# Optimization experiments

Measured on AMD Instinct MI355X. Metric: run time of the kernel, lower is better.

Reference implementation:

```python
import jax, jax.numpy as jnp
import numpy as np

BATCH, SEQ, DIM = 4, 4096, 1024


def setup_inputs() -> dict:
    key = jax.random.key(0)
    ks = jax.random.split(key, 7)
    return {
        "x": jax.random.normal(ks[0], (BATCH, SEQ, DIM), dtype=jnp.float32),
        "phazor_re": jax.random.normal(ks[1], (DIM,), dtype=jnp.float32),
        "phazor_im": jax.random.normal(ks[2], (DIM,), dtype=jnp.float32),
        "phazor_init_re": jax.random.normal(ks[3], (DIM,), dtype=jnp.float32),
        "phazor_init_im": jax.random.normal(ks[4], (DIM,), dtype=jnp.float32),
        "last_conv_re": jax.random.normal(ks[5], (BATCH, DIM), dtype=jnp.float32),
        "last_conv_im": jax.random.normal(ks[6], (BATCH, DIM), dtype=jnp.float32),
    }


def reference(x, phazor_re, phazor_im, phazor_init_re, phazor_init_im,
              last_conv_re, last_conv_im):
    L = x.shape[1]
    phazor_p = phazor_re + 1j * phazor_im                      # raw param (dim,)
    phazor_init = phazor_init_re + 1j * phazor_init_im          # (dim,)
    last_conv = last_conv_re + 1j * last_conv_im                # (batch, dim)

    mag = jnp.abs(phazor_p)
    phazor = phazor_p / mag * jnp.exp(-mag)                     # (dim,) |phazor|<1
    t = jnp.arange(L)[:, None]                                  # (L,1)
    phazor_prog = jnp.power(phazor[None, :], t)                 # (L, dim) = phazor^t
    filt = phazor_prog * phazor_init[None, :]                   # (L, dim)

    filt_fft = jnp.fft.fft(filt, n=2 * L, axis=0)               # (2L, dim)
    x_fft = jnp.fft.fft(x.astype(jnp.complex64), n=2 * L, axis=1)  # (B, 2L, dim)
    conv = jnp.fft.ifft(filt_fft[None] * x_fft, axis=1)[:, :L]  # (B, L, dim)

    # add decayed initial state: last_conv * phazor^(t+1)
    conv = conv + last_conv[:, None, :] * phazor_prog[None] * phazor[None, None, :]
    return conv.real
```

## Files before the change

kernel.cpp:

```cpp
#include <hip/hip_runtime.h>


#define BB 4
#define LL 4096
#define DD 1024
#define CHUNK 16
#define KK (LL / CHUNK)

__device__ __forceinline__ void phazor_of(float pr, float pi, float& ar, float& ai) {
    float mag = sqrtf(pr * pr + pi * pi);
    float s = expf(-mag) / mag;
    ar = pr * s;
    ai = pi * s;
}

__global__ __launch_bounds__(256, 4) void spiral_pass1(
    const float* __restrict__ x,
    const float* __restrict__ p_re, const float* __restrict__ p_im,
    const float* __restrict__ in_re, const float* __restrict__ in_im,
    float2* __restrict__ S)
{
    int tid = blockIdx.x * 256 + threadIdx.x;
    int dq = tid & (DD / 4 - 1);
    int k  = (tid >> 8) & (KK - 1);
    int b  = tid >> 16;
    int d0 = dq * 4;

    float4 prv = *(const float4*)(p_re + d0);
    float4 piv = *(const float4*)(p_im + d0);
    float4 brv = *(const float4*)(in_re + d0);
    float4 biv = *(const float4*)(in_im + d0);
    float ar[4], ai[4];
    float br[4] = {brv.x, brv.y, brv.z, brv.w};
    float bi[4] = {biv.x, biv.y, biv.z, biv.w};
    {
        float prs[4] = {prv.x, prv.y, prv.z, prv.w};
        float pis[4] = {piv.x, piv.y, piv.z, piv.w};
#pragma unroll
        for (int q = 0; q < 4; ++q) phazor_of(prs[q], pis[q], ar[q], ai[q]);
    }

    float sr[4] = {0.f, 0.f, 0.f, 0.f};
    float si[4] = {0.f, 0.f, 0.f, 0.f};
    const float* xp = x + ((size_t)(b * LL + k * CHUNK) * DD + d0);

#pragma unroll
    for (int t0 = 0; t0 < CHUNK; t0 += 8) {
        float4 xv[8];
#pragma unroll
        for (int j = 0; j < 8; ++j)
            xv[j] = *(const float4*)(xp + (size_t)(t0 + j) * DD);
#pragma unroll
        for (int j = 0; j < 8; ++j) {
            float xs[4] = {xv[j].x, xv[j].y, xv[j].z, xv[j].w};
#pragma unroll
            for (int q = 0; q < 4; ++q) {
                float nr = fmaf(ar[q], sr[q], fmaf(-ai[q], si[q], br[q] * xs[q]));
                float ni = fmaf(ar[q], si[q], fmaf( ai[q], sr[q], bi[q] * xs[q]));
                sr[q] = nr; si[q] = ni;
            }
        }
    }

    float2* Sp = S + ((size_t)(b * KK + k) * DD + d0);
#pragma unroll
    for (int q = 0; q < 4; ++q) Sp[q] = make_float2(sr[q], si[q]);
}

__global__ __launch_bounds__(256) void spiral_pass2(
    const float* __restrict__ p_re, const float* __restrict__ p_im,
    const float* __restrict__ lc_re, const float* __restrict__ lc_im,
    const float2* __restrict__ S,
    float2* __restrict__ C0)
{
    int tid = blockIdx.x * 256 + threadIdx.x;
    int d = tid & (DD - 1);
    int b = tid >> 10;

    float ar, ai;
    phazor_of(p_re[d], p_im[d], ar, ai);
    float qr = ar, qi = ai;
#pragma unroll
    for (int i = 0; i < 4; ++i) {
        float nr = qr * qr - qi * qi;
        float ni = 2.f * qr * qi;
        qr = nr; qi = ni;
    }

    const float2* Sp = S  + (size_t)b * KK * DD + d;
    float2*       Cp = C0 + (size_t)b * KK * DD + d;

    float cr = lc_re[b * DD + d];
    float ci = lc_im[b * DD + d];

    float2 buf[8];
#pragma unroll
    for (int j = 0; j < 8; ++j) buf[j] = Sp[(size_t)j * DD];

    for (int k = 0; k < KK; k += 8) {
#pragma unroll
        for (int j = 0; j < 8; ++j) {
            Cp[(size_t)(k + j) * DD] = make_float2(cr, ci);
            float2 s = buf[j];
            int kn = k + j + 8;
            buf[j] = Sp[(size_t)(kn < KK ? kn : KK - 1) * DD];
            float nr = fmaf(qr, cr, fmaf(-qi, ci, s.x));
            float ni = fmaf(qr, ci, fmaf( qi, cr, s.y));
            cr = nr; ci = ni;
        }
    }
}

__global__ __launch_bounds__(256, 4) void spiral_pass3(
    const float* __restrict__ x,
    const float* __restrict__ p_re, const float* __restrict__ p_im,
    const float* __restrict__ in_re, const float* __restrict__ in_im,
    const float2* __restrict__ C0,
    float* __restrict__ out)
{
    int tid = blockIdx.x * 256 + threadIdx.x;
    int dq = tid & (DD / 4 - 1);
    int k  = (tid >> 8) & (KK - 1);
    int b  = tid >> 16;
    int d0 = dq * 4;

    float4 prv = *(const float4*)(p_re + d0);
    float4 piv = *(const float4*)(p_im + d0);
    float4 brv = *(const float4*)(in_re + d0);
    float4 biv = *(const float4*)(in_im + d0);
    float ar[4], ai[4];
    float br[4] = {brv.x, brv.y, brv.z, brv.w};
    float bi[4] = {biv.x, biv.y, biv.z, biv.w};
    {
        float prs[4] = {prv.x, prv.y, prv.z, prv.w};
        float pis[4] = {piv.x, piv.y, piv.z, piv.w};
#pragma unroll
        for (int q = 0; q < 4; ++q) phazor_of(prs[q], pis[q], ar[q], ai[q]);
    }

    float cr[4], ci[4];
    const float2* Cp = C0 + ((size_t)(b * KK + k) * DD + d0);
#pragma unroll
    for (int q = 0; q < 4; ++q) { float2 c = Cp[q]; cr[q] = c.x; ci[q] = c.y; }

    const size_t base = (size_t)(b * LL + k * CHUNK) * DD + d0;
    const float* xp = x + base;
    float* op = out + base;

#pragma unroll
    for (int t0 = 0; t0 < CHUNK; t0 += 8) {
        float4 xv[8];
#pragma unroll
        for (int j = 0; j < 8; ++j)
            xv[j] = *(const float4*)(xp + (size_t)(t0 + j) * DD);
#pragma unroll
        for (int j = 0; j < 8; ++j) {
            float xs[4] = {xv[j].x, xv[j].y, xv[j].z, xv[j].w};
            float os[4];
#pragma unroll
            for (int q = 0; q < 4; ++q) {
                float nr = fmaf(ar[q], cr[q], fmaf(-ai[q], ci[q], br[q] * xs[q]));
                float ni = fmaf(ar[q], ci[q], fmaf( ai[q], cr[q], bi[q] * xs[q]));
                cr[q] = nr; ci[q] = ni;
                os[q] = nr;
            }
            *(float4*)(op + (size_t)(t0 + j) * DD) = make_float4(os[0], os[1], os[2], os[3]);
        }
    }
}

extern "C" void kernel_launch(void* const* d_in, const int* in_sizes, int n_in,
                              void* d_out, int out_size, void* d_ws, size_t ws_size,
                              hipStream_t stream) {
    const float* x      = (const float*)d_in[0];
    const float* p_re   = (const float*)d_in[1];
    const float* p_im   = (const float*)d_in[2];
    const float* pin_re = (const float*)d_in[3];
    const float* pin_im = (const float*)d_in[4];
    const float* lc_re  = (const float*)d_in[5];
    const float* lc_im  = (const float*)d_in[6];
    float* out = (float*)d_out;

    float2* S  = (float2*)d_ws;
    float2* C0 = S + (size_t)BB * KK * DD;

    const int threads13 = BB * KK * (DD / 4);
    dim3 blk(256);
    dim3 grid13(threads13 / 256);
    dim3 grid2((BB * DD) / 256);

    spiral_pass1<<<grid13, blk, 0, stream>>>(x, p_re, p_im, pin_re, pin_im, S);
    spiral_pass2<<<grid2,  blk, 0, stream>>>(p_re, p_im, lc_re, lc_im, S, C0);
    spiral_pass3<<<grid13, blk, 0, stream>>>(x, p_re, p_im, pin_re, pin_im, C0, out);
}
```

Before: 158.6 us.

## Split serial chunk-carry scan into two-level segmented scan with fixup in pass 3

The single serial pass-2 scan over 256 chunks per (batch, dim) is replaced by a two-level scan. Segments of 32 chunks are scanned in parallel from a zero carry, then a short kernel chains the 8 segment carries. Pass 3 reconstructs each chunk's true carry by multiplying the segment carry by a power of the phazor computed through binary exponentiation. This exposes more parallelism in the latency-bound middle stage, at the cost of an extra launch, extra workspace traffic and some per-thread complex arithmetic in pass 3.

```diff
diff --git a/kernel.cpp b/kernel.cpp
--- a/kernel.cpp
+++ b/kernel.cpp
@@ -5,7 +5,9 @@
 #define LL 4096
 #define DD 1024
 #define CHUNK 16
-#define KK (LL / CHUNK)
+#define KK 256
+#define SEG 32
+#define NSEG 8
 
 __device__ __forceinline__ void phazor_of(float pr, float pi, float& ar, float& ai) {
     float mag = sqrtf(pr * pr + pi * pi);
@@ -14,7 +16,13 @@
     ai = pi * s;
 }
 
-__global__ __launch_bounds__(256, 4) void spiral_pass1(
+__device__ __forceinline__ void csq(float& r, float& i) {
+    float nr = r * r - i * i;
+    i = 2.f * r * i;
+    r = nr;
+}
+
+__global__ __launch_bounds__(256, 4) void spiral_p1(
     const float* __restrict__ x,
     const float* __restrict__ p_re, const float* __restrict__ p_im,
     const float* __restrict__ in_re, const float* __restrict__ in_im,
@@ -67,55 +75,80 @@
     for (int q = 0; q < 4; ++q) Sp[q] = make_float2(sr[q], si[q]);
 }
 
-__global__ __launch_bounds__(256) void spiral_pass2(
-    const float* __restrict__ p_re, const float* __restrict__ p_im,
-    const float* __restrict__ lc_re, const float* __restrict__ lc_im,
+__global__ __launch_bounds__(128) void spiral_p2a(
+    const float* __restrict__ p_re, const float* __restrict__ p_im,
     const float2* __restrict__ S,
-    float2* __restrict__ C0)
-{
-    int tid = blockIdx.x * 256 + threadIdx.x;
-    int d = tid & (DD - 1);
-    int b = tid >> 10;
-
-    float ar, ai;
-    phazor_of(p_re[d], p_im[d], ar, ai);
-    float qr = ar, qi = ai;
-#pragma unroll
-    for (int i = 0; i < 4; ++i) {
-        float nr = qr * qr - qi * qi;
-        float ni = 2.f * qr * qi;
-        qr = nr; qi = ni;
-    }
-
-    const float2* Sp = S  + (size_t)b * KK * DD + d;
-    float2*       Cp = C0 + (size_t)b * KK * DD + d;
-
-    float cr = lc_re[b * DD + d];
-    float ci = lc_im[b * DD + d];
+    float2* __restrict__ R, float2* __restrict__ T)
+{
+    int gt  = blockIdx.x * 128 + threadIdx.x;
+    int d   = gt & (DD - 1);
+    int seg = (gt >> 10) & (NSEG - 1);
+    int bb  = gt >> 13;
+
+    float qr, qi;
+    phazor_of(p_re[d], p_im[d], qr, qi);
+#pragma unroll
+    for (int i = 0; i < 4; ++i) csq(qr, qi);
+
+    const int kk0 = seg * SEG;
+    const float2* Sc = S + ((size_t)bb * KK * DD + d);
+    float2*       Rc = R + ((size_t)bb * KK * DD + d);
 
     float2 buf[8];
 #pragma unroll
-    for (int j = 0; j < 8; ++j) buf[j] = Sp[(size_t)j * DD];
-
-    for (int k = 0; k < KK; k += 8) {
+    for (int j = 0; j < 8; ++j) buf[j] = Sc[(size_t)(kk0 + j) * DD];
+
+    float cr = 0.f, ci = 0.f;
+    for (int i = 0; i < SEG; i += 8) {
 #pragma unroll
         for (int j = 0; j < 8; ++j) {
-            Cp[(size_t)(k + j) * DD] = make_float2(cr, ci);
+            Rc[(size_t)(kk0 + i + j) * DD] = make_float2(cr, ci);
             float2 s = buf[j];
-            int kn = k + j + 8;
-            buf[j] = Sp[(size_t)(kn < KK ? kn : KK - 1) * DD];
+            int kn = i + j + 8;
+            buf[j] = Sc[(size_t)(kk0 + (kn < SEG ? kn : SEG - 1)) * DD];
             float nr = fmaf(qr, cr, fmaf(-qi, ci, s.x));
             float ni = fmaf(qr, ci, fmaf( qi, cr, s.y));
             cr = nr; ci = ni;
         }
     }
-}
-
-__global__ __launch_bounds__(256, 4) void spiral_pass3(
+    T[((size_t)bb * NSEG + seg) * DD + d] = make_float2(cr, ci);
+}
+
+__global__ __launch_bounds__(128) void spiral_p2b(
+    const float* __restrict__ p_re, const float* __restrict__ p_im,
+    const float* __restrict__ lc_re, const float* __restrict__ lc_im,
+    const float2* __restrict__ T,
+    float2* __restrict__ segC)
+{
+    int gt = blockIdx.x * 128 + threadIdx.x;
+    int d  = gt & (DD - 1);
+    int bb = gt >> 10;
+
+    float qr, qi;
+    phazor_of(p_re[d], p_im[d], qr, qi);
+#pragma unroll
+    for (int i = 0; i < 9; ++i) csq(qr, qi);
+
+    float2 tb[NSEG];
+#pragma unroll
+    for (int s = 0; s < NSEG; ++s) tb[s] = T[((size_t)bb * NSEG + s) * DD + d];
+
+    float cr = lc_re[bb * DD + d];
+    float ci = lc_im[bb * DD + d];
+#pragma unroll
+    for (int s = 0; s < NSEG; ++s) {
+        segC[((size_t)bb * NSEG + s) * DD + d] = make_float2(cr, ci);
+        float nr = fmaf(qr, cr, fmaf(-qi, ci, tb[s].x));
+        float ni = fmaf(qr, ci, fmaf( qi, cr, tb[s].y));
+        cr = nr; ci = ni;
+    }
+}
+
+__global__ __launch_bounds__(256, 4) void spiral_p3(
     const float* __restrict__ x,
     const float* __restrict__ p_re, const float* __restrict__ p_im,
     const float* __restrict__ in_re, const float* __restrict__ in_im,
-    const float2* __restrict__ C0,
+    const float2* __restrict__ R, const float2* __restrict__ segC,
     float* __restrict__ out)
 {
     int tid = blockIdx.x * 256 + threadIdx.x;
@@ -123,6 +156,8 @@
     int k  = (tid >> 8) & (KK - 1);
     int b  = tid >> 16;
     int d0 = dq * 4;
+    int rel = k & (SEG - 1);
+    int seg = k >> 5;
 
     float4 prv = *(const float4*)(p_re + d0);
     float4 piv = *(const float4*)(p_im + d0);
@@ -139,9 +174,31 @@
     }
 
     float cr[4], ci[4];
-    const float2* Cp = C0 + ((size_t)(b * KK + k) * DD + d0);
-#pragma unroll
-    for (int q = 0; q < 4; ++q) { float2 c = Cp[q]; cr[q] = c.x; ci[q] = c.y; }
+    {
+        const float2* Rp = R    + ((size_t)(b * KK + k) * DD + d0);
+        const float2* Gp = segC + ((size_t)(b * NSEG + seg) * DD + d0);
+#pragma unroll
+        for (int q = 0; q < 4; ++q) {
+            float qdr = ar[q], qdi = ai[q];
+#pragma unroll
+            for (int i = 0; i < 4; ++i) csq(qdr, qdi);
+            float pr = 1.f, pi = 0.f;
+            float bpr = qdr, bpi = qdi;
+#pragma unroll
+            for (int bit = 0; bit < 5; ++bit) {
+                if ((rel >> bit) & 1) {
+                    float nr = pr * bpr - pi * bpi;
+                    pi = pr * bpi + pi * bpr;
+                    pr = nr;
+                }
+                csq(bpr, bpi);
+            }
+            float2 r = Rp[q];
+            float2 g = Gp[q];
+            cr[q] = r.x + pr * g.x - pi * g.y;
+            ci[q] = r.y + pr * g.y + pi * g.x;
+        }
+    }
 
     const size_t base = (size_t)(b * LL + k * CHUNK) * DD + d0;
     const float* xp = x + base;
@@ -181,15 +238,14 @@
     const float* lc_im  = (const float*)d_in[6];
     float* out = (float*)d_out;
 
-    float2* S  = (float2*)d_ws;
-    float2* C0 = S + (size_t)BB * KK * DD;
-
-    const int threads13 = BB * KK * (DD / 4);
-    dim3 blk(256);
-    dim3 grid13(threads13 / 256);
-    dim3 grid2((BB * DD) / 256);
-
-    spiral_pass1<<<grid13, blk, 0, stream>>>(x, p_re, p_im, pin_re, pin_im, S);
-    spiral_pass2<<<grid2,  blk, 0, stream>>>(p_re, p_im, lc_re, lc_im, S, C0);
-    spiral_pass3<<<grid13, blk, 0, stream>>>(x, p_re, p_im, pin_re, pin_im, C0, out);
-}
+    char* ws = (char*)d_ws;
+    float2* S    = (float2*)(ws);
+    float2* R    = (float2*)(ws + (size_t)8  * 1024 * 1024);
+    float2* T    = (float2*)(ws + (size_t)16 * 1024 * 1024);
+    float2* segC = (float2*)(ws + (size_t)16 * 1024 * 1024 + 256 * 1024);
+
+    spiral_p1 <<<dim3(1024), dim3(256), 0, stream>>>(x, p_re, p_im, pin_re, pin_im, S);
+    spiral_p2a<<<dim3(256),  dim3(128), 0, stream>>>(p_re, p_im, S, R, T);
+    spiral_p2b<<<dim3(32),   dim3(128), 0, stream>>>(p_re, p_im, lc_re, lc_im, T, segC);
+    spiral_p3 <<<dim3(1024), dim3(256), 0, stream>>>(x, p_re, p_im, pin_re, pin_im, R, segC, out);
+}
```

Result: faster. 142.8 us (-10.0%).
